# Kernel tuning notes

Hardware: AMD Instinct MI355X
Metric: run time of the kernel (lower is better)

Reference implementation:

```python
import math
import jax, jax.numpy as jnp
import numpy as np

B, S, HID, H, NREL = 4, 512, 1024, 16, 64
D = HID // H  # per-head size = 64, must equal relation embedding dim


def setup_inputs() -> dict:
    key = jax.random.key(0)
    ks = jax.random.split(key, 12)
    w = lambda k, shape: jax.random.normal(k, shape, jnp.float32) * 0.02
    return {
        "q_in": jax.random.normal(ks[0], (B, S, HID), jnp.float32),
        "k_in": jax.random.normal(ks[1], (B, S, HID), jnp.float32),
        "v_in": jax.random.normal(ks[2], (B, S, HID), jnp.float32),
        "mask": jax.random.randint(ks[3], (B, 1, S, S), 0, NREL),
        "Wq": w(ks[4], (HID, HID)), "bq": jnp.zeros((HID,), jnp.float32),
        "Wk": w(ks[5], (HID, HID)), "bk": jnp.zeros((HID,), jnp.float32),
        "Wv": w(ks[6], (HID, HID)), "bv": jnp.zeros((HID,), jnp.float32),
        "Wo": w(ks[7], (HID, HID)), "bo": jnp.zeros((HID,), jnp.float32),
        "rel_k_table": w(ks[8], (NREL, D)),
        "rel_v_table": w(ks[9], (NREL, D)),
    }


def reference(q_in, k_in, v_in, mask, Wq, bq, Wk, bk, Wv, bv, Wo, bo,
              rel_k_table, rel_v_table):
    def proj(x, W, b):  # [B,S,HID] -> [B,H,S,D]
        return (x @ W.T + b).reshape(B, S, H, D).transpose(0, 2, 1, 3)

    q = proj(q_in, Wq, bq)
    k = proj(k_in, Wk, bk)
    v = proj(v_in, Wv, bv)

    ids = mask[:, 0]                      # [B,S,S] relation ids
    rel_k = rel_k_table[ids]              # [B,S,S,D]
    rel_v = rel_v_table[ids]              # [B,S,S,D]

    scores = jnp.einsum('bhqd,bhkd->bhqk', q, k)
    scores = scores + jnp.einsum('bhqd,bqkd->bhqk', q, rel_k) / 4.0
    scores = scores / math.sqrt(float(D))

    bias = (1.0 - (mask > 0).astype(scores.dtype)) * -10000.0  # [B,1,S,S]
    probs = jax.nn.softmax(scores + bias, axis=-1)             # [B,H,S,S]

    out = jnp.einsum('bhqk,bhkd->bhqd', probs, v)
    out = out + 0.25 * jnp.einsum('bhqk,bqkd->bhqd', probs, rel_v)
    out = out.transpose(0, 2, 1, 3).reshape(B, S, HID)
    return out @ Wo.T + bo
```

## Files before the change

kernel.cpp:

```cpp
#include <hip/hip_runtime.h>


typedef __attribute__((ext_vector_type(8))) short bf16x8 __attribute__((may_alias));
typedef __attribute__((ext_vector_type(4))) float f32x4;

__device__ __forceinline__ short f2bf(float x) {
    unsigned u = __float_as_uint(x);
    u += 0x7fff + ((u >> 16) & 1);
    return (short)(u >> 16);
}

__device__ __forceinline__ void async16(void* lds, const void* g) {
    __builtin_amdgcn_global_load_lds(
        (const __attribute__((address_space(1))) void*)g,
        (__attribute__((address_space(3))) void*)lds, 16, 0, 0);
}

__global__ __launch_bounds__(256)
void cast_all(const float* __restrict__ x0, const float* __restrict__ x1, const float* __restrict__ x2,
              const float* __restrict__ w0, const float* __restrict__ w1,
              const float* __restrict__ w2, const float* __restrict__ w3,
              short* __restrict__ y0, short* __restrict__ y1, short* __restrict__ y2,
              short* __restrict__ u0, short* __restrict__ u1,
              short* __restrict__ u2, short* __restrict__ u3)
{
    size_t i = (size_t)blockIdx.x * 256 + threadIdx.x;
    const float* src; short* dst; size_t off;
    if (i < 3u*524288u) {
        int s = (int)(i / 524288u); off = i % 524288u;
        src = s == 0 ? x0 : (s == 1 ? x1 : x2);
        dst = s == 0 ? y0 : (s == 1 ? y1 : y2);
    } else {
        size_t j = i - 3u*524288u;
        int s = (int)(j / 262144u); off = j % 262144u;
        src = s == 0 ? w0 : (s == 1 ? w1 : (s == 2 ? w2 : w3));
        dst = s == 0 ? u0 : (s == 1 ? u1 : (s == 2 ? u2 : u3));
    }
    float4 f = ((const float4*)src)[off];
    short4 o; o.x = f2bf(f.x); o.y = f2bf(f.y); o.z = f2bf(f.z); o.w = f2bf(f.w);
    ((short4*)dst)[off] = o;
}

__global__ __launch_bounds__(256)
void gemm12864(const short* __restrict__ A0, const short* __restrict__ A1, const short* __restrict__ A2,
               const short* __restrict__ B0, const short* __restrict__ B1, const short* __restrict__ B2,
               const float* __restrict__ c0, const float* __restrict__ c1, const float* __restrict__ c2,
               void* __restrict__ O0, void* __restrict__ O1, void* __restrict__ O2,
               int mode)
{
    __shared__ short ldsw[2 * 12288];

    const int z = blockIdx.z;
    const short* A    = z == 0 ? A0 : (z == 1 ? A1 : A2);
    const short* Bm   = z == 0 ? B0 : (z == 1 ? B1 : B2);
    const float* bias = z == 0 ? c0 : (z == 1 ? c1 : c2);
    void*        O    = z == 0 ? O0 : (z == 1 ? O1 : O2);

    const int t = threadIdx.x;
    const int lane = t & 63, w = t >> 6;
    const int wr = w >> 1, wc = w & 1;
    const int quad = lane >> 4, cl = lane & 15;
    const int rowBase = blockIdx.y * 128;
    const int colBase = blockIdx.x * 64;
    const int gl = ((lane & 7) - (lane >> 3)) & 7;

    f32x4 acc[4][2];
#pragma unroll
    for (int i = 0; i < 4; ++i)
#pragma unroll
        for (int j = 0; j < 2; ++j) acc[i][j] = (f32x4){0.f, 0.f, 0.f, 0.f};

    const int rstage = w * 8 + (lane >> 3);
    const short* Ag = A  + (size_t)(rowBase + rstage) * 1024 + gl * 8;
    const short* Bg = Bm + (size_t)(colBase + rstage) * 1024 + gl * 8;

    {
        short* Als = ldsw;
        short* Bls = ldsw + 8192;
#pragma unroll
        for (int i = 0; i < 4; ++i)
            async16(&Als[(i * 32 + w * 8) * 64], Ag + (size_t)i * 32 * 1024);
#pragma unroll
        for (int i = 0; i < 2; ++i)
            async16(&Bls[(i * 32 + w * 8) * 64], Bg + (size_t)i * 32 * 1024);
    }

    for (int it = 0; it < 16; ++it) {
        const int cur = it & 1;
        __syncthreads();
        if (it < 15) {
            short* Als = ldsw + (cur ^ 1) * 12288;
            short* Bls = Als + 8192;
            const int k0 = (it + 1) * 64;
#pragma unroll
            for (int i = 0; i < 4; ++i)
                async16(&Als[(i * 32 + w * 8) * 64], Ag + (size_t)i * 32 * 1024 + k0);
#pragma unroll
            for (int i = 0; i < 2; ++i)
                async16(&Bls[(i * 32 + w * 8) * 64], Bg + (size_t)i * 32 * 1024 + k0);
        }
        const short* Als = ldsw + cur * 12288;
        const short* Bls = Als + 8192;
#pragma unroll
        for (int kk = 0; kk < 2; ++kk) {
            bf16x8 a[4], b[2];
#pragma unroll
            for (int mi = 0; mi < 4; ++mi) {
                int r = wr * 64 + mi * 16 + cl;
                int s = (kk * 4 + quad + r) & 7;
                a[mi] = *(const bf16x8*)&Als[r * 64 + s * 8];
            }
#pragma unroll
            for (int ni = 0; ni < 2; ++ni) {
                int r = wc * 32 + ni * 16 + cl;
                int s = (kk * 4 + quad + r) & 7;
                b[ni] = *(const bf16x8*)&Bls[r * 64 + s * 8];
            }
#pragma unroll
            for (int mi = 0; mi < 4; ++mi)
#pragma unroll
                for (int ni = 0; ni < 2; ++ni)
                    acc[mi][ni] = __builtin_amdgcn_mfma_f32_16x16x32_bf16(
                        a[mi], b[ni], acc[mi][ni], 0, 0, 0);
        }
    }

    if (mode == 0) {
#pragma unroll
        for (int mi = 0; mi < 4; ++mi)
#pragma unroll
            for (int ni = 0; ni < 2; ++ni) {
                int col = colBase + wc * 32 + ni * 16 + cl;
                float bv = bias[col];
#pragma unroll
                for (int reg = 0; reg < 4; ++reg) {
                    int row = rowBase + wr * 64 + mi * 16 + quad * 4 + reg;
                    ((float*)O)[(size_t)row * 1024 + col] = acc[mi][ni][reg] + bv;
                }
            }
        return;
    }

    __syncthreads();
    short* Tls = ldsw;
    if (z == 2) {
#pragma unroll
        for (int mi = 0; mi < 4; ++mi)
#pragma unroll
            for (int ni = 0; ni < 2; ++ni) {
                int d = wc * 32 + ni * 16 + cl;
                float bv = bias[colBase + d];
                short4 pk;
                pk.x = f2bf(acc[mi][ni][0] + bv);
                pk.y = f2bf(acc[mi][ni][1] + bv);
                pk.z = f2bf(acc[mi][ni][2] + bv);
                pk.w = f2bf(acc[mi][ni][3] + bv);
                int sl = wr * 64 + mi * 16 + quad * 4;
                *(short4*)&Tls[d * 136 + sl] = pk;
            }
        __syncthreads();
        int d = t >> 2, s0 = (t & 3) * 32;
        int bb = rowBase >> 9, sBase = rowBase & 511, hh = colBase >> 6;
        short* dst = (short*)O + (((size_t)(bb * 16 + hh) * 64 + d) << 9) + sBase + s0;
#pragma unroll
        for (int j = 0; j < 4; ++j)
            *(bf16x8*)(dst + j * 8) = *(const bf16x8*)&Tls[d * 136 + s0 + j * 8];
    } else {
#pragma unroll
        for (int mi = 0; mi < 4; ++mi)
#pragma unroll
            for (int ni = 0; ni < 2; ++ni) {
                int d = wc * 32 + ni * 16 + cl;
                float bv = bias[colBase + d];
#pragma unroll
                for (int reg = 0; reg < 4; ++reg) {
                    int sl = wr * 64 + mi * 16 + quad * 4 + reg;
                    Tls[sl * 72 + d] = f2bf(acc[mi][ni][reg] + bv);
                }
            }
        __syncthreads();
        int sl = t >> 1, half = t & 1;
        int bb = rowBase >> 9, sBase = rowBase & 511, hh = colBase >> 6;
        short* dst = (short*)O + (((size_t)(bb * 16 + hh) * 512 + sBase + sl) << 6) + half * 32;
#pragma unroll
        for (int j = 0; j < 4; ++j)
            *(bf16x8*)(dst + j * 8) = *(const bf16x8*)&Tls[sl * 72 + half * 32 + j * 8];
    }
}

#define AT_BINS 4352
#define AT_PST  8704
#define AT_TOT  11264

__global__ __launch_bounds__(64)
void attn_kernel(const short* __restrict__ qg, const short* __restrict__ kg,
                 const short* __restrict__ vtg, const int* __restrict__ mask,
                 const float* __restrict__ relk, const float* __restrict__ relv,
                 short* __restrict__ attn_b)
{
    __shared__ __align__(16) char pool[AT_TOT];
    float* qwr    = (float*)pool;
    float* bins   = (float*)(pool + AT_BINS);
    short* Pst    = (short*)(pool + AT_PST);
    short* binsBf = Pst;

    const int lane = threadIdx.x;
    const int quad = lane >> 4, cl = lane & 15;
    const int bid = blockIdx.x;
    const int bh = bid & 63, qbk = bid >> 6;
    const int b = bh >> 4, h = bh & 15, q0 = qbk * 16;

    const short* qbase = qg  + ((size_t)bh * 512 + q0) * 64;
    const short* kbase = kg  + (size_t)bh * 512 * 64;
    const short* vbase = vtg + (size_t)bh * 64 * 512;
    const int*   mb    = mask + (size_t)b * 512 * 512 + (size_t)q0 * 512;

    for (int i = lane; i < 16 * 68; i += 64) bins[i] = 0.f;

    bf16x8 qa0 = *(const bf16x8*)(qbase + cl * 64 + quad * 8);
    bf16x8 qa1 = *(const bf16x8*)(qbase + cl * 64 + 32 + quad * 8);

#pragma unroll
    for (int rt = 0; rt < 4; ++rt) {
        const float* kp = relk + (size_t)(rt * 16 + cl) * 64 + quad * 8;
        bf16x8 rb0, rb1;
#pragma unroll
        for (int j = 0; j < 8; ++j) rb0[j] = f2bf(kp[j]);
#pragma unroll
        for (int j = 0; j < 8; ++j) rb1[j] = f2bf(kp[32 + j]);
        f32x4 qr = (f32x4){0.f, 0.f, 0.f, 0.f};
        qr = __builtin_amdgcn_mfma_f32_16x16x32_bf16(qa0, rb0, qr, 0, 0, 0);
        qr = __builtin_amdgcn_mfma_f32_16x16x32_bf16(qa1, rb1, qr, 0, 0, 0);
#pragma unroll
        for (int reg = 0; reg < 4; ++reg)
            qwr[(quad * 4 + reg) * 68 + rt * 16 + cl] = qr[reg];
    }

    f32x4 oacc[4];
#pragma unroll
    for (int dt = 0; dt < 4; ++dt) oacc[dt] = (f32x4){0.f, 0.f, 0.f, 0.f};
    float lpart[4] = {0.f, 0.f, 0.f, 0.f};

    for (int c = 0; c < 8; ++c) {
        const int k0 = c * 64;
#pragma unroll
        for (int nt = 0; nt < 4; ++nt) {
            const int kidx = k0 + nt * 16 + cl;
            const short* kp = kbase + (size_t)kidx * 64 + quad * 8;
            bf16x8 kb0 = *(const bf16x8*)kp;
            bf16x8 kb1 = *(const bf16x8*)(kp + 32);
            f32x4 s = (f32x4){0.f, 0.f, 0.f, 0.f};
            s = __builtin_amdgcn_mfma_f32_16x16x32_bf16(qa0, kb0, s, 0, 0, 0);
            s = __builtin_amdgcn_mfma_f32_16x16x32_bf16(qa1, kb1, s, 0, 0, 0);
#pragma unroll
            for (int reg = 0; reg < 4; ++reg) {
                int q = quad * 4 + reg;
                int id = mb[q * 512 + kidx];
                float sc = (s[reg] + 0.25f * qwr[q * 68 + id]) * 0.125f;
                float p = (id == 0) ? 0.f : __expf(sc);
                lpart[reg] += p;
                atomicAdd(&bins[q * 68 + id], p);
                Pst[q * 72 + nt * 16 + cl] = f2bf(p);
            }
        }
        bf16x8 pa0 = *(const bf16x8*)&Pst[cl * 72 + quad * 8];
        bf16x8 pa1 = *(const bf16x8*)&Pst[cl * 72 + 32 + quad * 8];
#pragma unroll
        for (int dt = 0; dt < 4; ++dt) {
            const short* vp = vbase + (size_t)(dt * 16 + cl) * 512 + k0 + quad * 8;
            bf16x8 vb0 = *(const bf16x8*)vp;
            bf16x8 vb1 = *(const bf16x8*)(vp + 32);
            oacc[dt] = __builtin_amdgcn_mfma_f32_16x16x32_bf16(pa0, vb0, oacc[dt], 0, 0, 0);
            oacc[dt] = __builtin_amdgcn_mfma_f32_16x16x32_bf16(pa1, vb1, oacc[dt], 0, 0, 0);
        }
    }

    float invq[4];
#pragma unroll
    for (int reg = 0; reg < 4; ++reg) {
        float l = lpart[reg];
#pragma unroll
        for (int m = 8; m >= 1; m >>= 1) l += __shfl_xor(l, m);
        invq[reg] = 1.0f / l;
    }

    {
        int q = lane >> 2, r0 = (lane & 3) * 16;
#pragma unroll
        for (int j = 0; j < 4; ++j) {
            float4 f = *(const float4*)&bins[q * 68 + r0 + j * 4];
            short4 o;
            o.x = f2bf(f.x); o.y = f2bf(f.y); o.z = f2bf(f.z); o.w = f2bf(f.w);
            *(short4*)&binsBf[q * 72 + r0 + j * 4] = o;
        }
    }

    bf16x8 ba0 = *(const bf16x8*)&binsBf[cl * 72 + quad * 8];
    bf16x8 ba1 = *(const bf16x8*)&binsBf[cl * 72 + 32 + quad * 8];
#pragma unroll
    for (int dt = 0; dt < 4; ++dt) {
        const float* rp = relv + (size_t)(quad * 8) * 64 + dt * 16 + cl;
        bf16x8 rv0, rv1;
#pragma unroll
        for (int j = 0; j < 8; ++j) rv0[j] = f2bf(rp[j * 64]);
#pragma unroll
        for (int j = 0; j < 8; ++j) rv1[j] = f2bf(rp[2048 + j * 64]);
        f32x4 racc = (f32x4){0.f, 0.f, 0.f, 0.f};
        racc = __builtin_amdgcn_mfma_f32_16x16x32_bf16(ba0, rv0, racc, 0, 0, 0);
        racc = __builtin_amdgcn_mfma_f32_16x16x32_bf16(ba1, rv1, racc, 0, 0, 0);
#pragma unroll
        for (int reg = 0; reg < 4; ++reg) {
            int q = quad * 4 + reg;
            float val = (oacc[dt][reg] + 0.25f * racc[reg]) * invq[reg];
            attn_b[(size_t)(b * 512 + q0 + q) * 1024 + h * 64 + dt * 16 + cl] = f2bf(val);
        }
    }
}

extern "C" void kernel_launch(void* const* d_in, const int* in_sizes, int n_in,
                              void* d_out, int out_size, void* d_ws, size_t ws_size,
                              hipStream_t stream)
{
    const float* q_in = (const float*)d_in[0];
    const float* k_in = (const float*)d_in[1];
    const float* v_in = (const float*)d_in[2];
    const int*   mask = (const int*)d_in[3];
    const float* Wq   = (const float*)d_in[4];
    const float* bq   = (const float*)d_in[5];
    const float* Wk   = (const float*)d_in[6];
    const float* bk   = (const float*)d_in[7];
    const float* Wv   = (const float*)d_in[8];
    const float* bv   = (const float*)d_in[9];
    const float* Wo   = (const float*)d_in[10];
    const float* bo   = (const float*)d_in[11];
    const float* relk = (const float*)d_in[12];
    const float* relv = (const float*)d_in[13];

    char* ws = (char*)d_ws;
    short* qb     = (short*)(ws);
    short* kb     = (short*)(ws + (4u  << 20));
    short* vt     = (short*)(ws + (8u  << 20));
    short* attn_b = (short*)(ws + (12u << 20));
    short* Xq     = (short*)(ws + (16u << 20));
    short* Xk     = (short*)(ws + (20u << 20));
    short* Xv     = (short*)(ws + (24u << 20));
    short* Wqb    = (short*)(ws + (28u << 20));
    short* Wkb    = (short*)(ws + (30u << 20));
    short* Wvb    = (short*)(ws + (32u << 20));
    short* Wob    = (short*)(ws + (34u << 20));

    cast_all<<<10240, 256, 0, stream>>>(q_in, k_in, v_in, Wq, Wk, Wv, Wo,
                                        Xq, Xk, Xv, Wqb, Wkb, Wvb, Wob);

    gemm12864<<<dim3(16, 16, 3), 256, 0, stream>>>(
        Xq, Xk, Xv, Wqb, Wkb, Wvb, bq, bk, bv, qb, kb, vt, 1);

    attn_kernel<<<dim3(2048), 64, 0, stream>>>(qb, kb, vt, mask, relk, relv, attn_b);

    gemm12864<<<dim3(16, 16, 1), 256, 0, stream>>>(
        attn_b, attn_b, attn_b, Wob, Wob, Wob, bo, bo, bo,
        (void*)d_out, (void*)d_out, (void*)d_out, 0);
}
```

Baseline: 239.0 us.

## Split attention key range across two waves and prefetch K/V/mask per chunk

```diff
diff --git a/kernel.cpp b/kernel.cpp
--- a/kernel.cpp
+++ b/kernel.cpp
@@ -188,23 +188,23 @@
     }
 }
 
-#define AT_BINS 4352
-#define AT_PST  8704
-#define AT_TOT  11264
-
-__global__ __launch_bounds__(64)
+#define AT_BINS  4352
+#define AT_PST   13056
+#define AT_OPART 17664
+#define AT_LACC  26368
+#define AT_TOT   26496
+
+__global__ __launch_bounds__(128)
 void attn_kernel(const short* __restrict__ qg, const short* __restrict__ kg,
                  const short* __restrict__ vtg, const int* __restrict__ mask,
                  const float* __restrict__ relk, const float* __restrict__ relv,
                  short* __restrict__ attn_b)
 {
     __shared__ __align__(16) char pool[AT_TOT];
-    float* qwr    = (float*)pool;
-    float* bins   = (float*)(pool + AT_BINS);
-    short* Pst    = (short*)(pool + AT_PST);
-    short* binsBf = Pst;
-
-    const int lane = threadIdx.x;
+    float* qwr  = (float*)pool;
+    float* Lacc = (float*)(pool + AT_LACC);
+
+    const int t = threadIdx.x, lane = t & 63, w = t >> 6;
     const int quad = lane >> 4, cl = lane & 15;
     const int bid = blockIdx.x;
     const int bh = bid & 63, qbk = bid >> 6;
@@ -215,13 +215,18 @@
     const short* vbase = vtg + (size_t)bh * 64 * 512;
     const int*   mb    = mask + (size_t)b * 512 * 512 + (size_t)q0 * 512;
 
+    float* bins  = (float*)(pool + AT_BINS  + w * 4352);
+    short* Pst   = (short*)(pool + AT_PST   + w * 2304);
+    float* Opart = (float*)(pool + AT_OPART + w * 4352);
+
     for (int i = lane; i < 16 * 68; i += 64) bins[i] = 0.f;
 
     bf16x8 qa0 = *(const bf16x8*)(qbase + cl * 64 + quad * 8);
     bf16x8 qa1 = *(const bf16x8*)(qbase + cl * 64 + 32 + quad * 8);
 
 #pragma unroll
-    for (int rt = 0; rt < 4; ++rt) {
+    for (int rt2 = 0; rt2 < 2; ++rt2) {
+        const int rt = w * 2 + rt2;
         const float* kp = relk + (size_t)(rt * 16 + cl) * 64 + quad * 8;
         bf16x8 rb0, rb1;
 #pragma unroll
@@ -235,27 +240,44 @@
         for (int reg = 0; reg < 4; ++reg)
             qwr[(quad * 4 + reg) * 68 + rt * 16 + cl] = qr[reg];
     }
+    __syncthreads();
 
     f32x4 oacc[4];
 #pragma unroll
     for (int dt = 0; dt < 4; ++dt) oacc[dt] = (f32x4){0.f, 0.f, 0.f, 0.f};
     float lpart[4] = {0.f, 0.f, 0.f, 0.f};
 
-    for (int c = 0; c < 8; ++c) {
-        const int k0 = c * 64;
+    for (int c = 0; c < 4; ++c) {
+        const int k0 = w * 256 + c * 64;
+        bf16x8 kb[8], vb[8];
+        int idv[16];
 #pragma unroll
         for (int nt = 0; nt < 4; ++nt) {
-            const int kidx = k0 + nt * 16 + cl;
-            const short* kp = kbase + (size_t)kidx * 64 + quad * 8;
-            bf16x8 kb0 = *(const bf16x8*)kp;
-            bf16x8 kb1 = *(const bf16x8*)(kp + 32);
+            const short* kp = kbase + (size_t)(k0 + nt * 16 + cl) * 64 + quad * 8;
+            kb[nt * 2]     = *(const bf16x8*)kp;
+            kb[nt * 2 + 1] = *(const bf16x8*)(kp + 32);
+        }
+#pragma unroll
+        for (int dt = 0; dt < 4; ++dt) {
+            const short* vp = vbase + (size_t)(dt * 16 + cl) * 512 + k0 + quad * 8;
+            vb[dt * 2]     = *(const bf16x8*)vp;
+            vb[dt * 2 + 1] = *(const bf16x8*)(vp + 32);
+        }
+#pragma unroll
+        for (int nt = 0; nt < 4; ++nt)
+#pragma unroll
+            for (int reg = 0; reg < 4; ++reg)
+                idv[nt * 4 + reg] = mb[(quad * 4 + reg) * 512 + k0 + nt * 16 + cl];
+
+#pragma unroll
+        for (int nt = 0; nt < 4; ++nt) {
             f32x4 s = (f32x4){0.f, 0.f, 0.f, 0.f};
-            s = __builtin_amdgcn_mfma_f32_16x16x32_bf16(qa0, kb0, s, 0, 0, 0);
-            s = __builtin_amdgcn_mfma_f32_16x16x32_bf16(qa1, kb1, s, 0, 0, 0);
+            s = __builtin_amdgcn_mfma_f32_16x16x32_bf16(qa0, kb[nt * 2],     s, 0, 0, 0);
+            s = __builtin_amdgcn_mfma_f32_16x16x32_bf16(qa1, kb[nt * 2 + 1], s, 0, 0, 0);
 #pragma unroll
             for (int reg = 0; reg < 4; ++reg) {
                 int q = quad * 4 + reg;
-                int id = mb[q * 512 + kidx];
+                int id = idv[nt * 4 + reg];
                 float sc = (s[reg] + 0.25f * qwr[q * 68 + id]) * 0.125f;
                 float p = (id == 0) ? 0.f : __expf(sc);
                 lpart[reg] += p;
@@ -267,38 +289,47 @@
         bf16x8 pa1 = *(const bf16x8*)&Pst[cl * 72 + 32 + quad * 8];
 #pragma unroll
         for (int dt = 0; dt < 4; ++dt) {
-            const short* vp = vbase + (size_t)(dt * 16 + cl) * 512 + k0 + quad * 8;
-            bf16x8 vb0 = *(const bf16x8*)vp;
-            bf16x8 vb1 = *(const bf16x8*)(vp + 32);
-            oacc[dt] = __builtin_amdgcn_mfma_f32_16x16x32_bf16(pa0, vb0, oacc[dt], 0, 0, 0);
-            oacc[dt] = __builtin_amdgcn_mfma_f32_16x16x32_bf16(pa1, vb1, oacc[dt], 0, 0, 0);
-        }
-    }
+            oacc[dt] = __builtin_amdgcn_mfma_f32_16x16x32_bf16(pa0, vb[dt * 2],     oacc[dt], 0, 0, 0);
+            oacc[dt] = __builtin_amdgcn_mfma_f32_16x16x32_bf16(pa1, vb[dt * 2 + 1], oacc[dt], 0, 0, 0);
+        }
+    }
+
+#pragma unroll
+    for (int reg = 0; reg < 4; ++reg) {
+        int q = quad * 4 + reg;
+#pragma unroll
+        for (int dt = 0; dt < 4; ++dt)
+            Opart[q * 68 + dt * 16 + cl] = oacc[dt][reg];
+        float lsum = lpart[reg];
+#pragma unroll
+        for (int m = 8; m >= 1; m >>= 1) lsum += __shfl_xor(lsum, m);
+        if (cl == 0) Lacc[w * 16 + q] = lsum;
+    }
+    __syncthreads();
+
+    const float* b0 = (const float*)(pool + AT_BINS);
+    const float* b1 = (const float*)(pool + AT_BINS + 4352);
+    bf16x8 ba0, ba1;
+#pragma unroll
+    for (int j = 0; j < 8; ++j)
+        ba0[j] = f2bf(b0[cl * 68 + quad * 8 + j] + b1[cl * 68 + quad * 8 + j]);
+#pragma unroll
+    for (int j = 0; j < 8; ++j)
+        ba1[j] = f2bf(b0[cl * 68 + 32 + quad * 8 + j] + b1[cl * 68 + 32 + quad * 8 + j]);
 
     float invq[4];
 #pragma unroll
     for (int reg = 0; reg < 4; ++reg) {
-        float l = lpart[reg];
-#pragma unroll
-        for (int m = 8; m >= 1; m >>= 1) l += __shfl_xor(l, m);
-        invq[reg] = 1.0f / l;
-    }
-
-    {
-        int q = lane >> 2, r0 = (lane & 3) * 16;
-#pragma unroll
-        for (int j = 0; j < 4; ++j) {
-            float4 f = *(const float4*)&bins[q * 68 + r0 + j * 4];
-            short4 o;
-            o.x = f2bf(f.x); o.y = f2bf(f.y); o.z = f2bf(f.z); o.w = f2bf(f.w);
-            *(short4*)&binsBf[q * 72 + r0 + j * 4] = o;
-        }
-    }
-
-    bf16x8 ba0 = *(const bf16x8*)&binsBf[cl * 72 + quad * 8];
-    bf16x8 ba1 = *(const bf16x8*)&binsBf[cl * 72 + 32 + quad * 8];
-#pragma unroll
-    for (int dt = 0; dt < 4; ++dt) {
+        int q = quad * 4 + reg;
+        invq[reg] = 1.0f / (Lacc[q] + Lacc[16 + q]);
+    }
+
+    const float* Op0 = (const float*)(pool + AT_OPART);
+    const float* Op1 = (const float*)(pool + AT_OPART + 4352);
+
+#pragma unroll
+    for (int dt2 = 0; dt2 < 2; ++dt2) {
+        const int dt = w * 2 + dt2;
         const float* rp = relv + (size_t)(quad * 8) * 64 + dt * 16 + cl;
         bf16x8 rv0, rv1;
 #pragma unroll
@@ -311,8 +342,9 @@
 #pragma unroll
         for (int reg = 0; reg < 4; ++reg) {
             int q = quad * 4 + reg;
-            float val = (oacc[dt][reg] + 0.25f * racc[reg]) * invq[reg];
-            attn_b[(size_t)(b * 512 + q0 + q) * 1024 + h * 64 + dt * 16 + cl] = f2bf(val);
+            int d = dt * 16 + cl;
+            float val = (Op0[q * 68 + d] + Op1[q * 68 + d] + 0.25f * racc[reg]) * invq[reg];
+            attn_b[(size_t)(b * 512 + q0 + q) * 1024 + h * 64 + d] = f2bf(val);
         }
     }
 }
@@ -355,7 +387,7 @@
     gemm12864<<<dim3(16, 16, 3), 256, 0, stream>>>(
         Xq, Xk, Xv, Wqb, Wkb, Wvb, bq, bk, bv, qb, kb, vt, 1);
 
-    attn_kernel<<<dim3(2048), 64, 0, stream>>>(qb, kb, vt, mask, relk, relv, attn_b);
+    attn_kernel<<<dim3(2048), 128, 0, stream>>>(qb, kb, vt, mask, relk, relv, attn_b);
 
     gemm12864<<<dim3(16, 16, 1), 256, 0, stream>>>(
         attn_b, attn_b, attn_b, Wob, Wob, Wob, bo, bo, bo,
```

Measured after the change: 246.5 us. 3.1% more time.

## Split q·relK into separate kernel and keep P in registers via fp16 MFMA transpose

Applied to the files above, without the earlier changes.

```diff
diff --git a/kernel.cpp b/kernel.cpp
--- a/kernel.cpp
+++ b/kernel.cpp
@@ -3,11 +3,17 @@
 
 typedef __attribute__((ext_vector_type(8))) short bf16x8 __attribute__((may_alias));
 typedef __attribute__((ext_vector_type(4))) float f32x4;
+typedef __attribute__((ext_vector_type(4))) _Float16 f16x4 __attribute__((may_alias));
 
 __device__ __forceinline__ short f2bf(float x) {
     unsigned u = __float_as_uint(x);
     u += 0x7fff + ((u >> 16) & 1);
     return (short)(u >> 16);
+}
+__device__ __forceinline__ short f2h(float x) {
+    union { _Float16 h; short s; } u;
+    u.h = (_Float16)x;
+    return u.s;
 }
 
 __device__ __forceinline__ void async16(void* lds, const void* g) {
@@ -151,10 +157,10 @@
                 int d = wc * 32 + ni * 16 + cl;
                 float bv = bias[colBase + d];
                 short4 pk;
-                pk.x = f2bf(acc[mi][ni][0] + bv);
-                pk.y = f2bf(acc[mi][ni][1] + bv);
-                pk.z = f2bf(acc[mi][ni][2] + bv);
-                pk.w = f2bf(acc[mi][ni][3] + bv);
+                pk.x = f2h(acc[mi][ni][0] + bv);
+                pk.y = f2h(acc[mi][ni][1] + bv);
+                pk.z = f2h(acc[mi][ni][2] + bv);
+                pk.w = f2h(acc[mi][ni][3] + bv);
                 int sl = wr * 64 + mi * 16 + quad * 4;
                 *(short4*)&Tls[d * 136 + sl] = pk;
             }
@@ -188,21 +194,47 @@
     }
 }
 
-#define AT_BINS 4352
-#define AT_PST  8704
-#define AT_TOT  11264
+__global__ __launch_bounds__(64)
+void qrel_kernel(const short* __restrict__ qg, const float* __restrict__ relk,
+                 float* __restrict__ qrelg)
+{
+    const int lane = threadIdx.x;
+    const int quad = lane >> 4, cl = lane & 15;
+    const int bid = blockIdx.x;
+    const int bh = bid & 63, qbk = bid >> 6;
+    const int q0 = qbk * 16;
+
+    const short* qbase = qg + ((size_t)bh * 512 + q0) * 64;
+    float* out = qrelg + ((size_t)bh * 512 + q0) * 64;
+
+    bf16x8 qa0 = *(const bf16x8*)(qbase + cl * 64 + quad * 8);
+    bf16x8 qa1 = *(const bf16x8*)(qbase + cl * 64 + 32 + quad * 8);
+
+#pragma unroll
+    for (int rt = 0; rt < 4; ++rt) {
+        const float* kp = relk + (size_t)(rt * 16 + cl) * 64 + quad * 8;
+        bf16x8 rb0, rb1;
+#pragma unroll
+        for (int j = 0; j < 8; ++j) rb0[j] = f2bf(kp[j]);
+#pragma unroll
+        for (int j = 0; j < 8; ++j) rb1[j] = f2bf(kp[32 + j]);
+        f32x4 qr = (f32x4){0.f, 0.f, 0.f, 0.f};
+        qr = __builtin_amdgcn_mfma_f32_16x16x32_bf16(qa0, rb0, qr, 0, 0, 0);
+        qr = __builtin_amdgcn_mfma_f32_16x16x32_bf16(qa1, rb1, qr, 0, 0, 0);
+#pragma unroll
+        for (int reg = 0; reg < 4; ++reg)
+            out[(size_t)(quad * 4 + reg) * 64 + rt * 16 + cl] = qr[reg];
+    }
+}
 
 __global__ __launch_bounds__(64)
 void attn_kernel(const short* __restrict__ qg, const short* __restrict__ kg,
-                 const short* __restrict__ vtg, const int* __restrict__ mask,
-                 const float* __restrict__ relk, const float* __restrict__ relv,
+                 const _Float16* __restrict__ vtg, const int* __restrict__ mask,
+                 const float* __restrict__ qrelg, const float* __restrict__ relv,
                  short* __restrict__ attn_b)
 {
-    __shared__ __align__(16) char pool[AT_TOT];
-    float* qwr    = (float*)pool;
-    float* bins   = (float*)(pool + AT_BINS);
-    short* Pst    = (short*)(pool + AT_PST);
-    short* binsBf = Pst;
+    __shared__ __align__(16) float bins[16 * 68];
+    __shared__ __align__(16) short binsBf[16 * 72];
 
     const int lane = threadIdx.x;
     const int quad = lane >> 4, cl = lane & 15;
@@ -210,31 +242,20 @@
     const int bh = bid & 63, qbk = bid >> 6;
     const int b = bh >> 4, h = bh & 15, q0 = qbk * 16;
 
-    const short* qbase = qg  + ((size_t)bh * 512 + q0) * 64;
-    const short* kbase = kg  + (size_t)bh * 512 * 64;
-    const short* vbase = vtg + (size_t)bh * 64 * 512;
-    const int*   mb    = mask + (size_t)b * 512 * 512 + (size_t)q0 * 512;
+    const short*    qbase = qg  + ((size_t)bh * 512 + q0) * 64;
+    const short*    kbase = kg  + (size_t)bh * 512 * 64;
+    const _Float16* vbase = vtg + (size_t)bh * 64 * 512;
+    const int*      mb    = mask + (size_t)b * 512 * 512 + (size_t)q0 * 512;
+    const float*    qrb   = qrelg + ((size_t)bh * 512 + q0) * 64;
 
     for (int i = lane; i < 16 * 68; i += 64) bins[i] = 0.f;
 
     bf16x8 qa0 = *(const bf16x8*)(qbase + cl * 64 + quad * 8);
     bf16x8 qa1 = *(const bf16x8*)(qbase + cl * 64 + 32 + quad * 8);
 
-#pragma unroll
-    for (int rt = 0; rt < 4; ++rt) {
-        const float* kp = relk + (size_t)(rt * 16 + cl) * 64 + quad * 8;
-        bf16x8 rb0, rb1;
-#pragma unroll
-        for (int j = 0; j < 8; ++j) rb0[j] = f2bf(kp[j]);
-#pragma unroll
-        for (int j = 0; j < 8; ++j) rb1[j] = f2bf(kp[32 + j]);
-        f32x4 qr = (f32x4){0.f, 0.f, 0.f, 0.f};
-        qr = __builtin_amdgcn_mfma_f32_16x16x32_bf16(qa0, rb0, qr, 0, 0, 0);
-        qr = __builtin_amdgcn_mfma_f32_16x16x32_bf16(qa1, rb1, qr, 0, 0, 0);
-#pragma unroll
-        for (int reg = 0; reg < 4; ++reg)
-            qwr[(quad * 4 + reg) * 68 + rt * 16 + cl] = qr[reg];
-    }
+    f16x4 idB;
+#pragma unroll
+    for (int j = 0; j < 4; ++j) idB[j] = (quad * 4 + j == cl) ? (_Float16)1.0f : (_Float16)0.0f;
 
     f32x4 oacc[4];
 #pragma unroll
@@ -243,6 +264,14 @@
 
     for (int c = 0; c < 8; ++c) {
         const int k0 = c * 64;
+        f16x4 vb[4][4];
+#pragma unroll
+        for (int nt = 0; nt < 4; ++nt)
+#pragma unroll
+            for (int dt = 0; dt < 4; ++dt)
+                vb[nt][dt] = *(const f16x4*)(vbase + (size_t)(dt * 16 + cl) * 512
+                                             + k0 + nt * 16 + quad * 4);
+
 #pragma unroll
         for (int nt = 0; nt < 4; ++nt) {
             const int kidx = k0 + nt * 16 + cl;
@@ -252,26 +281,27 @@
             f32x4 s = (f32x4){0.f, 0.f, 0.f, 0.f};
             s = __builtin_amdgcn_mfma_f32_16x16x32_bf16(qa0, kb0, s, 0, 0, 0);
             s = __builtin_amdgcn_mfma_f32_16x16x32_bf16(qa1, kb1, s, 0, 0, 0);
+
+            f16x4 pA;
 #pragma unroll
             for (int reg = 0; reg < 4; ++reg) {
                 int q = quad * 4 + reg;
                 int id = mb[q * 512 + kidx];
-                float sc = (s[reg] + 0.25f * qwr[q * 68 + id]) * 0.125f;
+                float sc = (s[reg] + 0.25f * qrb[q * 64 + id]) * 0.125f;
                 float p = (id == 0) ? 0.f : __expf(sc);
                 lpart[reg] += p;
                 atomicAdd(&bins[q * 68 + id], p);
-                Pst[q * 72 + nt * 16 + cl] = f2bf(p);
-            }
-        }
-        bf16x8 pa0 = *(const bf16x8*)&Pst[cl * 72 + quad * 8];
-        bf16x8 pa1 = *(const bf16x8*)&Pst[cl * 72 + 32 + quad * 8];
-#pragma unroll
-        for (int dt = 0; dt < 4; ++dt) {
-            const short* vp = vbase + (size_t)(dt * 16 + cl) * 512 + k0 + quad * 8;
-            bf16x8 vb0 = *(const bf16x8*)vp;
-            bf16x8 vb1 = *(const bf16x8*)(vp + 32);
-            oacc[dt] = __builtin_amdgcn_mfma_f32_16x16x32_bf16(pa0, vb0, oacc[dt], 0, 0, 0);
-            oacc[dt] = __builtin_amdgcn_mfma_f32_16x16x32_bf16(pa1, vb1, oacc[dt], 0, 0, 0);
+                pA[reg] = (_Float16)p;
+            }
+            f32x4 tD = __builtin_amdgcn_mfma_f32_16x16x16f16(pA, idB,
+                         (f32x4){0.f, 0.f, 0.f, 0.f}, 0, 0, 0);
+            f16x4 paT;
+#pragma unroll
+            for (int j = 0; j < 4; ++j) paT[j] = (_Float16)tD[j];
+#pragma unroll
+            for (int dt = 0; dt < 4; ++dt)
+                oacc[dt] = __builtin_amdgcn_mfma_f32_16x16x16f16(paT, vb[nt][dt],
+                                                                 oacc[dt], 0, 0, 0);
         }
     }
 
@@ -337,17 +367,18 @@
     const float* relv = (const float*)d_in[13];
 
     char* ws = (char*)d_ws;
-    short* qb     = (short*)(ws);
-    short* kb     = (short*)(ws + (4u  << 20));
-    short* vt     = (short*)(ws + (8u  << 20));
-    short* attn_b = (short*)(ws + (12u << 20));
-    short* Xq     = (short*)(ws + (16u << 20));
-    short* Xk     = (short*)(ws + (20u << 20));
-    short* Xv     = (short*)(ws + (24u << 20));
-    short* Wqb    = (short*)(ws + (28u << 20));
-    short* Wkb    = (short*)(ws + (30u << 20));
-    short* Wvb    = (short*)(ws + (32u << 20));
-    short* Wob    = (short*)(ws + (34u << 20));
+    short*     qb     = (short*)(ws);
+    short*     kb     = (short*)(ws + (4u  << 20));
+    _Float16*  vt     = (_Float16*)(ws + (8u << 20));
+    short*     attn_b = (short*)(ws + (12u << 20));
+    short*     Xq     = (short*)(ws + (16u << 20));
+    short*     Xk     = (short*)(ws + (20u << 20));
+    short*     Xv     = (short*)(ws + (24u << 20));
+    short*     Wqb    = (short*)(ws + (28u << 20));
+    short*     Wkb    = (short*)(ws + (30u << 20));
+    short*     Wvb    = (short*)(ws + (32u << 20));
+    short*     Wob    = (short*)(ws + (34u << 20));
+    float*     qrelg  = (float*)(ws + (36u << 20));
 
     cast_all<<<10240, 256, 0, stream>>>(q_in, k_in, v_in, Wq, Wk, Wv, Wo,
                                         Xq, Xk, Xv, Wqb, Wkb, Wvb, Wob);
@@ -355,7 +386,9 @@
     gemm12864<<<dim3(16, 16, 3), 256, 0, stream>>>(
         Xq, Xk, Xv, Wqb, Wkb, Wvb, bq, bk, bv, qb, kb, vt, 1);
 
-    attn_kernel<<<dim3(2048), 64, 0, stream>>>(qb, kb, vt, mask, relk, relv, attn_b);
+    qrel_kernel<<<dim3(2048), 64, 0, stream>>>(qb, relk, qrelg);
+
+    attn_kernel<<<dim3(2048), 64, 0, stream>>>(qb, kb, vt, mask, qrelg, relv, attn_b);
 
     gemm12864<<<dim3(16, 16, 1), 256, 0, stream>>>(
         attn_b, attn_b, attn_b, Wob, Wob, Wob, bo, bo, bo,
```

After: 243.1 us. About the same (+1.7%).
